# Kernel tuning notes

Hardware: AMD Instinct MI355X
Metric: run time of the kernel (lower is better)

The kernel has to match this reference:

```python
import jax, jax.numpy as jnp
import numpy as np

EPS = 1e-6
ALPHA = 0.1
BETA = 0.25


def setup_inputs() -> dict:
    key = jax.random.key(0)
    k1, k2, k3 = jax.random.split(key, 3)
    B, C, D = 4096, 256, 128
    x = jax.random.normal(k1, (B, D), dtype=jnp.float32)
    prev_q = jax.random.normal(k2, (B, D), dtype=jnp.float32)
    codes = jax.random.normal(k3, (1, C, D), dtype=jnp.float32)
    return {"x": x, "prev_q": prev_q, "codes": codes}


def compute_distance(x, codes):
    # x: (B, D); codes: (1, C, D) or (B, 1, D) -> (B, C) / (B, 1); metric='l2'
    return jnp.sum((x[:, None, :] - codes) ** 2, axis=-1)


def get_rotation_matrix(u, v, eps=EPS):
    # u: (B, D) normalized; v: (D,) normalized -> R: (B, D, D)
    B, D = u.shape
    uvT = u[:, :, None] * v[None, None, :]          # (B, D, D) = u v^T
    vuT = v[None, :, None] * u[:, None, :]          # (B, D, D) = v u^T
    A = uvT - vuT
    A2 = jnp.einsum('bik,bkj->bij', A, A)
    dot = jnp.einsum('bd,d->b', u, v)[:, None, None]
    I = jnp.eye(D, dtype=u.dtype)
    return I + A + A2 / (1.0 + dot + eps)


def reference(x, prev_q, codes):
    B, D = x.shape
    v = jnp.ones((D,), dtype=x.dtype) / jnp.sqrt(jnp.asarray(D, x.dtype))
    # F.normalize(prev_q, dim=-1, eps=1e-6)
    n = jnp.linalg.norm(prev_q, axis=-1, keepdims=True)
    u = prev_q / jnp.maximum(n, EPS)
    R = get_rotation_matrix(u, v)
    # x_canonical = R^T x
    x_canonical = jnp.einsum('bji,bj->bi', R, x)
    raw_distances = compute_distance(x_canonical, codes)        # (B, C)
    distances = raw_distances / D / ALPHA
    # eval path: argmin + gather
    indices = jnp.argmin(distances, axis=-1)                    # (B,)
    quantized_canonical = codes[0][indices]                     # (B, D)
    quantized = jnp.einsum('bij,bj->bi', R, quantized_canonical)
    loss_commit = compute_distance(x, jax.lax.stop_gradient(quantized)[:, None, :]).mean()
    loss_codebook = compute_distance(jax.lax.stop_gradient(x), quantized[:, None, :]).mean()
    loss = loss_commit + BETA * loss_codebook
    return quantized, indices, loss
```

## Files before the change

kernel.cpp:

```cpp
#include <hip/hip_runtime.h>

#define BD 4096
#define CD 256
#define DD 128
#define ROWS 8
#define CT 64
#define PAD 132

__global__ __launch_bounds__(256) void rq_fused(
    const float* __restrict__ x,
    const float* __restrict__ pq,
    const float* __restrict__ codes,
    float* __restrict__ out)
{
    __shared__ float xc_s[ROWS * PAD];
    __shared__ float code_s[CT * PAD];
    __shared__ float row_c[ROWS], row_s[ROWS], row_invn[ROWS];
    __shared__ int   row_idx[ROWS];
    __shared__ float loss_s[ROWS];

    const int tid  = threadIdx.x;
    const int wave = tid >> 6;
    const int lane = tid & 63;
    const int row0 = blockIdx.x * ROWS;
    const float INV_SQRT_D = 0.088388347648318447f;

    #pragma unroll
    for (int rr = 0; rr < 2; ++rr) {
        const int r = wave * 2 + rr;
        const size_t grow = (size_t)(row0 + r);
        const float2 xv = ((const float2*)(x  + grow * DD))[lane];
        const float2 pv = ((const float2*)(pq + grow * DD))[lane];
        float s0 = pv.x * pv.x + pv.y * pv.y;
        float s1 = pv.x + pv.y;
        float s2 = xv.x + xv.y;
        float s3 = pv.x * xv.x + pv.y * xv.y;
        #pragma unroll
        for (int m = 32; m > 0; m >>= 1) {
            s0 += __shfl_xor(s0, m);
            s1 += __shfl_xor(s1, m);
            s2 += __shfl_xor(s2, m);
            s3 += __shfl_xor(s3, m);
        }
        const float n    = sqrtf(s0);
        const float invn = 1.0f / fmaxf(n, 1e-6f);
        const float b = s2 * INV_SQRT_D;
        const float a = s3 * invn;
        const float c = s1 * invn * INV_SQRT_D;
        const float s = 1.0f / (1.0f + c + 1e-6f);
        const float au = -b + s * (c * b - a);
        const float av =  a + s * (c * a - b);
        const float ux = pv.x * invn, uy = pv.y * invn;
        xc_s[r * PAD + 2 * lane]     = xv.x + au * ux + av * INV_SQRT_D;
        xc_s[r * PAD + 2 * lane + 1] = xv.y + au * uy + av * INV_SQRT_D;
        if (lane == 0) { row_c[r] = c; row_s[r] = s; row_invn[r] = invn; }
    }
    __syncthreads();

    const int rg = tid >> 5;
    const int cg = tid & 31;
    float bestv0 = 3.4e38f;
    int   besti0 = 0;

    for (int t = 0; t < CD / CT; ++t) {
        const float4* src = ((const float4*)codes) + (size_t)t * (CT * DD / 4);
        #pragma unroll
        for (int k = 0; k < (CT * DD / 4) / 256; ++k) {
            const int f  = k * 256 + tid;
            const int cr = f >> 5, cc = f & 31;
            *(float4*)(code_s + cr * PAD + cc * 4) = src[f];
        }
        __syncthreads();

        float acc0 = 0.f, acc1 = 0.f;
        const float* xr = xc_s + rg * PAD;
        const float* ca = code_s + cg * PAD;
        const float* cb = code_s + (cg + 32) * PAD;
        #pragma unroll
        for (int d4 = 0; d4 < 32; ++d4) {
            const float4 xa = *(const float4*)(xr + d4 * 4);
            const float4 va = *(const float4*)(ca + d4 * 4);
            const float4 vb = *(const float4*)(cb + d4 * 4);
            float dx;
            dx = xa.x - va.x; acc0 = fmaf(dx, dx, acc0);
            dx = xa.y - va.y; acc0 = fmaf(dx, dx, acc0);
            dx = xa.z - va.z; acc0 = fmaf(dx, dx, acc0);
            dx = xa.w - va.w; acc0 = fmaf(dx, dx, acc0);
            dx = xa.x - vb.x; acc1 = fmaf(dx, dx, acc1);
            dx = xa.y - vb.y; acc1 = fmaf(dx, dx, acc1);
            dx = xa.z - vb.z; acc1 = fmaf(dx, dx, acc1);
            dx = xa.w - vb.w; acc1 = fmaf(dx, dx, acc1);
        }
        const int i0 = t * CT + cg;
        const int i1 = t * CT + cg + 32;
        if (acc0 < bestv0) { bestv0 = acc0; besti0 = i0; }
        if (acc1 < bestv0) { bestv0 = acc1; besti0 = i1; }
        __syncthreads();
    }
    #pragma unroll
    for (int m = 16; m > 0; m >>= 1) {
        const float ov0 = __shfl_xor(bestv0, m); const int oi0 = __shfl_xor(besti0, m);
        if (ov0 < bestv0 || (ov0 == bestv0 && oi0 < besti0)) { bestv0 = ov0; besti0 = oi0; }
    }
    if (cg == 0) {
        row_idx[rg] = besti0;
        out[(size_t)BD * DD + row0 + rg] = (float)besti0;
    }
    __syncthreads();

    {
        const int r = tid >> 5;
        const int g = tid & 31;
        const int qi = row_idx[r];
        const float invn = row_invn[r];
        const float c = row_c[r];
        const float s = row_s[r];
        const size_t grow = (size_t)(row0 + r);
        const float4 q0 = *(const float4*)(codes + (size_t)qi * DD + 4 * g);
        const float4 p0 = *(const float4*)(pq + grow * DD + 4 * g);
        float pd = p0.x * q0.x + p0.y * q0.y + p0.z * q0.z + p0.w * q0.w;
        float ws = q0.x + q0.y + q0.z + q0.w;
        #pragma unroll
        for (int m = 16; m > 0; m >>= 1) {
            pd += __shfl_xor(pd, m);
            ws += __shfl_xor(ws, m);
        }
        const float p = pd * invn;
        const float w = ws * INV_SQRT_D;
        const float bu =  w + s * (c * w - p);
        const float bv = -p + s * (c * p - w);
        float4 o0;
        o0.x = q0.x + bu * (p0.x * invn) + bv * INV_SQRT_D;
        o0.y = q0.y + bu * (p0.y * invn) + bv * INV_SQRT_D;
        o0.z = q0.z + bu * (p0.z * invn) + bv * INV_SQRT_D;
        o0.w = q0.w + bu * (p0.w * invn) + bv * INV_SQRT_D;
        *(float4*)(out + grow * DD + 4 * g) = o0;

        const float4 x0 = *(const float4*)(x + grow * DD + 4 * g);
        float ls = 0.f, dx;
        dx = x0.x - o0.x; ls = fmaf(dx, dx, ls);
        dx = x0.y - o0.y; ls = fmaf(dx, dx, ls);
        dx = x0.z - o0.z; ls = fmaf(dx, dx, ls);
        dx = x0.w - o0.w; ls = fmaf(dx, dx, ls);
        #pragma unroll
        for (int m = 16; m > 0; m >>= 1) ls += __shfl_xor(ls, m);
        if (g == 0) loss_s[r] = ls;
    }
    __syncthreads();
    if (tid == 0) {
        float tot = 0.f;
        #pragma unroll
        for (int r = 0; r < ROWS; ++r) tot += loss_s[r];
        atomicAdd(out + (size_t)BD * DD + BD, tot * (1.25f / (float)BD));
    }
}

extern "C" void kernel_launch(void* const* d_in, const int* in_sizes, int n_in,
                              void* d_out, int out_size, void* d_ws, size_t ws_size,
                              hipStream_t stream) {
    const float* xin   = (const float*)d_in[0];
    const float* prevq = (const float*)d_in[1];
    const float* codes = (const float*)d_in[2];
    float* out = (float*)d_out;
    hipMemsetAsync((void*)(out + (size_t)BD * DD + BD), 0, sizeof(float), stream);
    rq_fused<<<BD / ROWS, 256, 0, stream>>>(xin, prevq, codes, out);
}
```

Before: 87.34 us.

## Halve rows per block, register-prefetch code tiles, split dims across lanes

```diff
diff --git a/kernel.cpp b/kernel.cpp
--- a/kernel.cpp
+++ b/kernel.cpp
@@ -3,11 +3,12 @@
 #define BD 4096
 #define CD 256
 #define DD 128
-#define ROWS 8
-#define CT 64
+#define ROWS 4
+#define CT 32
+#define NT (CD / CT)
 #define PAD 132
 
-__global__ __launch_bounds__(256) void rq_fused(
+__global__ __launch_bounds__(256, 4) void rq_fused(
     const float* __restrict__ x,
     const float* __restrict__ pq,
     const float* __restrict__ codes,
@@ -17,17 +18,18 @@
     __shared__ float code_s[CT * PAD];
     __shared__ float row_c[ROWS], row_s[ROWS], row_invn[ROWS];
     __shared__ int   row_idx[ROWS];
+    __shared__ float red_v[ROWS * 4];
+    __shared__ int   red_i[ROWS * 4];
     __shared__ float loss_s[ROWS];
 
     const int tid  = threadIdx.x;
-    const int wave = tid >> 6;
+    const int wv   = tid >> 6;
     const int lane = tid & 63;
     const int row0 = blockIdx.x * ROWS;
     const float INV_SQRT_D = 0.088388347648318447f;
 
-    #pragma unroll
-    for (int rr = 0; rr < 2; ++rr) {
-        const int r = wave * 2 + rr;
+    {
+        const int r = wv;
         const size_t grow = (size_t)(row0 + r);
         const float2 xv = ((const float2*)(x  + grow * DD))[lane];
         const float2 pv = ((const float2*)(pq + grow * DD))[lane];
@@ -42,115 +44,124 @@
             s2 += __shfl_xor(s2, m);
             s3 += __shfl_xor(s3, m);
         }
-        const float n    = sqrtf(s0);
-        const float invn = 1.0f / fmaxf(n, 1e-6f);
+        const float invn = 1.0f / fmaxf(sqrtf(s0), 1e-6f);
         const float b = s2 * INV_SQRT_D;
         const float a = s3 * invn;
         const float c = s1 * invn * INV_SQRT_D;
         const float s = 1.0f / (1.0f + c + 1e-6f);
         const float au = -b + s * (c * b - a);
         const float av =  a + s * (c * a - b);
-        const float ux = pv.x * invn, uy = pv.y * invn;
-        xc_s[r * PAD + 2 * lane]     = xv.x + au * ux + av * INV_SQRT_D;
-        xc_s[r * PAD + 2 * lane + 1] = xv.y + au * uy + av * INV_SQRT_D;
+        xc_s[r * PAD + 2 * lane]     = xv.x + au * (pv.x * invn) + av * INV_SQRT_D;
+        xc_s[r * PAD + 2 * lane + 1] = xv.y + au * (pv.y * invn) + av * INV_SQRT_D;
         if (lane == 0) { row_c[r] = c; row_s[r] = s; row_invn[r] = invn; }
     }
-    __syncthreads();
 
-    const int rg = tid >> 5;
-    const int cg = tid & 31;
-    float bestv0 = 3.4e38f;
-    int   besti0 = 0;
+    const int lc  = lane & 7;
+    const int lcD = (lane >> 3) & 1;
+    const int lr  = lane >> 4;
+    float bestv = 3.4e38f;
+    int   besti = 0;
 
-    for (int t = 0; t < CD / CT; ++t) {
-        const float4* src = ((const float4*)codes) + (size_t)t * (CT * DD / 4);
+    float4 pf[4];
+    {
+        const float4* src = (const float4*)codes;
         #pragma unroll
-        for (int k = 0; k < (CT * DD / 4) / 256; ++k) {
-            const int f  = k * 256 + tid;
-            const int cr = f >> 5, cc = f & 31;
-            *(float4*)(code_s + cr * PAD + cc * 4) = src[f];
+        for (int k = 0; k < 4; ++k) pf[k] = src[k * 256 + tid];
+    }
+
+    for (int t = 0; t < NT; ++t) {
+        __syncthreads();
+        #pragma unroll
+        for (int k = 0; k < 4; ++k) {
+            const int f = k * 256 + tid;
+            *(float4*)(code_s + (f >> 5) * PAD + (f & 31) * 4) = pf[k];
         }
         __syncthreads();
+        if (t + 1 < NT) {
+            const float4* src = ((const float4*)codes) + (size_t)(t + 1) * (CT * DD / 4);
+            #pragma unroll
+            for (int k = 0; k < 4; ++k) pf[k] = src[k * 256 + tid];
+        }
 
+        const int cit = wv * 8 + lc;
+        const float* xr = xc_s   + lr  * PAD + lcD * 64;
+        const float* cr = code_s + cit * PAD + lcD * 64;
         float acc0 = 0.f, acc1 = 0.f;
-        const float* xr = xc_s + rg * PAD;
-        const float* ca = code_s + cg * PAD;
-        const float* cb = code_s + (cg + 32) * PAD;
         #pragma unroll
-        for (int d4 = 0; d4 < 32; ++d4) {
+        for (int d4 = 0; d4 < 16; ++d4) {
             const float4 xa = *(const float4*)(xr + d4 * 4);
-            const float4 va = *(const float4*)(ca + d4 * 4);
-            const float4 vb = *(const float4*)(cb + d4 * 4);
+            const float4 va = *(const float4*)(cr + d4 * 4);
             float dx;
             dx = xa.x - va.x; acc0 = fmaf(dx, dx, acc0);
-            dx = xa.y - va.y; acc0 = fmaf(dx, dx, acc0);
+            dx = xa.y - va.y; acc1 = fmaf(dx, dx, acc1);
             dx = xa.z - va.z; acc0 = fmaf(dx, dx, acc0);
-            dx = xa.w - va.w; acc0 = fmaf(dx, dx, acc0);
-            dx = xa.x - vb.x; acc1 = fmaf(dx, dx, acc1);
-            dx = xa.y - vb.y; acc1 = fmaf(dx, dx, acc1);
-            dx = xa.z - vb.z; acc1 = fmaf(dx, dx, acc1);
-            dx = xa.w - vb.w; acc1 = fmaf(dx, dx, acc1);
+            dx = xa.w - va.w; acc1 = fmaf(dx, dx, acc1);
         }
-        const int i0 = t * CT + cg;
-        const int i1 = t * CT + cg + 32;
-        if (acc0 < bestv0) { bestv0 = acc0; besti0 = i0; }
-        if (acc1 < bestv0) { bestv0 = acc1; besti0 = i1; }
-        __syncthreads();
+        float dsum = acc0 + acc1;
+        dsum += __shfl_xor(dsum, 8);
+        const int ci = t * CT + cit;
+        if (dsum < bestv) { bestv = dsum; besti = ci; }
     }
+
     #pragma unroll
-    for (int m = 16; m > 0; m >>= 1) {
-        const float ov0 = __shfl_xor(bestv0, m); const int oi0 = __shfl_xor(besti0, m);
-        if (ov0 < bestv0 || (ov0 == bestv0 && oi0 < besti0)) { bestv0 = ov0; besti0 = oi0; }
+    for (int m = 8; m > 0; m >>= 1) {
+        const float ov = __shfl_xor(bestv, m);
+        const int   oi = __shfl_xor(besti, m);
+        if (ov < bestv || (ov == bestv && oi < besti)) { bestv = ov; besti = oi; }
     }
-    if (cg == 0) {
-        row_idx[rg] = besti0;
-        out[(size_t)BD * DD + row0 + rg] = (float)besti0;
+    if ((lane & 15) == 0) { red_v[lr * 4 + wv] = bestv; red_i[lr * 4 + wv] = besti; }
+    __syncthreads();
+    if (tid < ROWS) {
+        float bv = red_v[tid * 4];
+        int   bi = red_i[tid * 4];
+        #pragma unroll
+        for (int w = 1; w < 4; ++w) {
+            const float ov = red_v[tid * 4 + w];
+            const int   oi = red_i[tid * 4 + w];
+            if (ov < bv || (ov == bv && oi < bi)) { bv = ov; bi = oi; }
+        }
+        row_idx[tid] = bi;
+        out[(size_t)BD * DD + row0 + tid] = (float)bi;
     }
     __syncthreads();
 
     {
-        const int r = tid >> 5;
-        const int g = tid & 31;
+        const int r = wv;
         const int qi = row_idx[r];
         const float invn = row_invn[r];
         const float c = row_c[r];
         const float s = row_s[r];
         const size_t grow = (size_t)(row0 + r);
-        const float4 q0 = *(const float4*)(codes + (size_t)qi * DD + 4 * g);
-        const float4 p0 = *(const float4*)(pq + grow * DD + 4 * g);
-        float pd = p0.x * q0.x + p0.y * q0.y + p0.z * q0.z + p0.w * q0.w;
-        float ws = q0.x + q0.y + q0.z + q0.w;
+        const float2 q = ((const float2*)(codes + (size_t)qi * DD))[lane];
+        const float2 p = ((const float2*)(pq + grow * DD))[lane];
+        float pd = p.x * q.x + p.y * q.y;
+        float ws = q.x + q.y;
         #pragma unroll
-        for (int m = 16; m > 0; m >>= 1) {
+        for (int m = 32; m > 0; m >>= 1) {
             pd += __shfl_xor(pd, m);
             ws += __shfl_xor(ws, m);
         }
-        const float p = pd * invn;
-        const float w = ws * INV_SQRT_D;
-        const float bu =  w + s * (c * w - p);
-        const float bv = -p + s * (c * p - w);
-        float4 o0;
-        o0.x = q0.x + bu * (p0.x * invn) + bv * INV_SQRT_D;
-        o0.y = q0.y + bu * (p0.y * invn) + bv * INV_SQRT_D;
-        o0.z = q0.z + bu * (p0.z * invn) + bv * INV_SQRT_D;
-        o0.w = q0.w + bu * (p0.w * invn) + bv * INV_SQRT_D;
-        *(float4*)(out + grow * DD + 4 * g) = o0;
+        const float pp = pd * invn;
+        const float w  = ws * INV_SQRT_D;
+        const float bu =  w + s * (c * w - pp);
+        const float bv = -pp + s * (c * pp - w);
+        float2 o;
+        o.x = q.x + bu * (p.x * invn) + bv * INV_SQRT_D;
+        o.y = q.y + bu * (p.y * invn) + bv * INV_SQRT_D;
+        ((float2*)(out + grow * DD))[lane] = o;
 
-        const float4 x0 = *(const float4*)(x + grow * DD + 4 * g);
-        float ls = 0.f, dx;
-        dx = x0.x - o0.x; ls = fmaf(dx, dx, ls);
-        dx = x0.y - o0.y; ls = fmaf(dx, dx, ls);
-        dx = x0.z - o0.z; ls = fmaf(dx, dx, ls);
-        dx = x0.w - o0.w; ls = fmaf(dx, dx, ls);
+        const float2 xv = ((const float2*)(x + grow * DD))[lane];
+        float dx = xv.x - o.x;
+        float ls = dx * dx;
+        dx = xv.y - o.y;
+        ls = fmaf(dx, dx, ls);
         #pragma unroll
-        for (int m = 16; m > 0; m >>= 1) ls += __shfl_xor(ls, m);
-        if (g == 0) loss_s[r] = ls;
+        for (int m = 32; m > 0; m >>= 1) ls += __shfl_xor(ls, m);
+        if (lane == 0) loss_s[r] = ls;
     }
     __syncthreads();
     if (tid == 0) {
-        float tot = 0.f;
-        #pragma unroll
-        for (int r = 0; r < ROWS; ++r) tot += loss_s[r];
+        const float tot = loss_s[0] + loss_s[1] + loss_s[2] + loss_s[3];
         atomicAdd(out + (size_t)BD * DD + BD, tot * (1.25f / (float)BD));
     }
 }
```

Measured after the change: 109.9 us. 25.8% more time.
